# Kernel optimization log

Measured on AMD Instinct MI355X. Metric: run time of the kernel, lower is better.

## Reference

```python
import jax, jax.numpy as jnp
import numpy as np

# single species, e3tb basis 1s+1p+1d
FLIST = [1, 3, 5]           # flistnorbs (spin_factor = 1 pre-doubling)
NORB = 9                    # full_basis_norb
SPIN = 2                    # spin_deg -> block doubled
A, E, K = 192, 3072, 4
P = 58                      # sum_{i<=j} iorb*jorb = 1+3+5+9+15+25


def setup_inputs() -> dict:
    key = jax.random.key(0)
    ks = jax.random.split(key, 6)
    return dict(
        orbpair_hopping=jax.random.normal(ks[0], (E, P), jnp.float32),
        orbpair_onsite=jax.random.normal(ks[1], (A, P), jnp.float32),
        R_matrix=jax.random.normal(ks[2], (A, SPIN * NORB, SPIN * NORB), jnp.float32) * 0.1,
        kpoints=jax.random.uniform(ks[3], (K, 3), jnp.float32),
        edge_cell_shift=jax.random.normal(ks[4], (E, 3), jnp.float32),
        edge_index=jax.random.randint(ks[5], (2, E), 0, A, jnp.int64),
    )


def _assemble(feats):
    """Scatter flat orbpair features into upper-triangular [*, NORB, NORB] blocks."""
    n = feats.shape[0]
    H = jnp.zeros((n, NORB, NORB), feats.dtype)
    offs = np.concatenate([[0], np.cumsum(FLIST)])
    p = 0
    for i in range(len(FLIST)):
        for j in range(i, len(FLIST)):
            io, jo = FLIST[i], FLIST[j]
            f = 0.5 if i == j else 1.0  # diagonal orbpairs get 0.5 (hermitianized later)
            H = H.at[:, offs[i]:offs[i] + io, offs[j]:offs[j] + jo].set(
                f * feats[:, p:p + io * jo].reshape(n, io, jo))
            p += io * jo
    return H


def _spin_double(H):
    # H[:, :, 0, :, 0] = H[:, :, 1, :, 1] = H  (kron with eye(2), interleaved layout)
    n = H.shape[0]
    return jnp.einsum('aij,st->aisjt', H, jnp.eye(2, dtype=H.dtype)).reshape(n, SPIN * NORB, SPIN * NORB)


def reference(orbpair_hopping, orbpair_onsite, R_matrix, kpoints, edge_cell_shift, edge_index):
    s = SPIN * NORB
    src, dst = edge_index[0], edge_index[1]

    onsite = _spin_double(_assemble(orbpair_onsite))      # [A, s, s]
    hop = _spin_double(_assemble(orbpair_hopping))        # [E, s, s]

    # rotate: R @ H @ R^T (gathered per-edge for hoppings)
    onsite = jnp.einsum('aip,apq,ajq->aij', R_matrix, onsite, R_matrix)
    hop = jnp.einsum('eip,epq,ejq->eij', R_matrix[src], hop, R_matrix[dst])

    # Bloch phases exp(-2*pi*i k.S) per (k, edge)
    phase = jnp.exp(-2j * jnp.pi * (kpoints @ edge_cell_shift.T)).astype(jnp.complex64)  # [K, E]

    contrib = hop[None].astype(jnp.complex64) * phase[:, :, None, None]  # [K, E, s, s]
    pair = src * A + dst
    blk = jax.vmap(lambda c: jax.ops.segment_sum(c, pair, num_segments=A * A))(contrib)
    blk = blk.reshape(K, A, A, s, s)

    idx = jnp.arange(A)
    blk = blk.at[:, idx, idx].add(onsite[None].astype(jnp.complex64))  # onsite on diag, all k

    Hk = blk.transpose(0, 1, 3, 2, 4).reshape(K, A * s, A * s)
    return Hk + jnp.conj(jnp.swapaxes(Hk, 1, 2))
```

## Files before the change

kernel.cpp:

```cpp
#include <hip/hip_runtime.h>

#define PFEAT 58
#define S18   18
#define ENT   324
#define MAXE  128
#define MAXA  256

__device__ __constant__ unsigned char c_row[PFEAT] = {
    0,0,0,0,0,0,0,0,0,
    1,1,1,2,2,2,3,3,3,
    1,1,1,1,1,2,2,2,2,2,3,3,3,3,3,
    4,4,4,4,4,5,5,5,5,5,6,6,6,6,6,7,7,7,7,7,8,8,8,8,8};
__device__ __constant__ unsigned char c_col[PFEAT] = {
    0,1,2,3,4,5,6,7,8,
    1,2,3,1,2,3,1,2,3,
    4,5,6,7,8,4,5,6,7,8,4,5,6,7,8,
    4,5,6,7,8,4,5,6,7,8,4,5,6,7,8,4,5,6,7,8,4,5,6,7,8};
__device__ __constant__ float c_fac[PFEAT] = {
    0.5f,1,1,1,1,1,1,1,1,
    0.5f,0.5f,0.5f,0.5f,0.5f,0.5f,0.5f,0.5f,0.5f,
    1,1,1,1,1,1,1,1,1,1,1,1,1,1,1,
    0.5f,0.5f,0.5f,0.5f,0.5f,0.5f,0.5f,0.5f,0.5f,0.5f,0.5f,0.5f,0.5f,
    0.5f,0.5f,0.5f,0.5f,0.5f,0.5f,0.5f,0.5f,0.5f,0.5f,0.5f,0.5f};

__device__ __forceinline__ bool detect_i64(const int* __restrict__ ei) {
    const uint2* p = (const uint2*)ei;
    unsigned acc = 0u;
#pragma unroll 8
    for (int m = 0; m < 64; ++m) acc |= p[m].y;
    return acc == 0u;
}

__device__ __forceinline__ int load_idx(const int* __restrict__ ei, int pos,
                                        bool is64, int A) {
    int v = is64 ? ei[2 * pos] : ei[pos];
    v = v < 0 ? 0 : (v >= A ? A - 1 : v);
    return v;
}

__device__ __forceinline__ void assemble_rotate(
    const float* __restrict__ feat, const float* __restrict__ Rs,
    const float* __restrict__ Rd, float* sH9, float* sRs, float* sRd,
    float* sT, float* sM, int t, int nthreads)
{
    for (int idx = t; idx < ENT; idx += nthreads) { sRs[idx] = Rs[idx]; sRd[idx] = Rd[idx]; }
    if (t < 81) sH9[t] = 0.f;
    __syncthreads();
    if (t < PFEAT) sH9[c_row[t] * 9 + c_col[t]] = c_fac[t] * feat[t];
    __syncthreads();

    for (int idx = t; idx < ENT; idx += nthreads) {
        const int pp = idx / S18, q = idx - pp * S18;
        const int i = pp >> 1, u = pp & 1;
        float acc = 0.f;
#pragma unroll
        for (int j = 0; j < 9; ++j)
            acc += sH9[i * 9 + j] * sRd[q * S18 + 2 * j + u];
        sT[idx] = acc;
    }
    __syncthreads();

    for (int idx = t; idx < ENT; idx += nthreads) {
        const int p = idx / S18, q = idx - p * S18;
        float acc = 0.f;
#pragma unroll
        for (int pp = 0; pp < S18; ++pp)
            acc += sRs[p * S18 + pp] * sT[pp * S18 + q];
        sM[idx] = acc;
    }
}


__global__ __launch_bounds__(128) void prep_kernel(
    const float* __restrict__ hop_feat, const float* __restrict__ ons_feat,
    const float* __restrict__ R, const int* __restrict__ ei,
    const float* __restrict__ kpts, const float* __restrict__ shift,
    float* __restrict__ hop_rot, float* __restrict__ hop_rotT,
    float* __restrict__ ons_rot, float* __restrict__ pcos,
    float* __restrict__ psin, int* __restrict__ offsets,
    int2* __restrict__ entries, int E, int A, int K, int hasT)
{
    __shared__ float sH9[81];
    __shared__ float sRs[ENT];
    __shared__ float sRd[ENT];
    __shared__ float sT[ENT];
    __shared__ float sM[ENT];
    __shared__ int   scnt[MAXA];
    __shared__ int   scur[MAXA];
    __shared__ int   sflag;

    const int item = blockIdx.x;
    const int t = threadIdx.x;
    if (t == 0) sflag = detect_i64(ei) ? 1 : 0;
    __syncthreads();
    const bool s64 = sflag != 0;

    if (item == E + A) {
        for (int a = t; a < A; a += 128) scnt[a] = 0;
        __syncthreads();
        for (int e = t; e < E; e += 128) {
            const int a = load_idx(ei, e, s64, A);
            const int b = load_idx(ei, E + e, s64, A);
            atomicAdd(&scnt[a], 1);
            atomicAdd(&scnt[b], 1);
        }
        __syncthreads();
        if (t == 0) {
            int acc = 0;
            for (int a = 0; a < A; ++a) { scur[a] = acc; offsets[a] = acc; acc += scnt[a]; }
            offsets[A] = acc;
        }
        __syncthreads();
        for (int e = t; e < E; e += 128) {
            const int a = load_idx(ei, e, s64, A);
            const int b = load_idx(ei, E + e, s64, A);
            const int p = atomicAdd(&scur[a], 1);
            entries[p] = make_int2(e, b);
            const int q = atomicAdd(&scur[b], 1);
            entries[q] = make_int2(e | (1 << 30), a);
        }
        return;
    }

    const float* feat; const float* Rs; const float* Rd; float* outp;
    if (item < E) {
        const int a_s = load_idx(ei, item, s64, A);
        const int a_d = load_idx(ei, E + item, s64, A);
        feat = hop_feat + (size_t)item * PFEAT;
        Rs = R + (size_t)a_s * ENT;
        Rd = R + (size_t)a_d * ENT;
        outp = hop_rot + (size_t)item * ENT;
        for (int k = t; k < K; k += 128) {
            const float dot = kpts[k * 3 + 0] * shift[3 * item + 0]
                            + kpts[k * 3 + 1] * shift[3 * item + 1]
                            + kpts[k * 3 + 2] * shift[3 * item + 2];
            float sv, cv;
            sincosf(-6.28318530717958647692f * dot, &sv, &cv);
            pcos[item * K + k] = cv;
            psin[item * K + k] = sv;
        }
    } else {
        const int a = item - E;
        feat = ons_feat + (size_t)a * PFEAT;
        Rs = R + (size_t)a * ENT;
        Rd = Rs;
        outp = ons_rot + (size_t)a * ENT;
    }

    assemble_rotate(feat, Rs, Rd, sH9, sRs, sRd, sT, sM, t, 128);
    __syncthreads();

    for (int idx = t; idx < ENT; idx += 128) outp[idx] = sM[idx];
    if (item < E && hasT) {
        float* outpT = hop_rotT + (size_t)item * ENT;
        for (int idx = t; idx < ENT; idx += 128) {
            const int p = idx / S18, q = idx - p * S18;
            outpT[idx] = sM[q * S18 + p];
        }
    }
}

__global__ __launch_bounds__(384) void writer_cols_kernel(
    const float* __restrict__ hop_rot,
    const float* __restrict__ hop_rotT,
    const float* __restrict__ ons_rot,
    const int*   __restrict__ offsets,
    const int2*  __restrict__ entries,
    const float* __restrict__ pcos,
    float* __restrict__ outf,
    int A, int K, long long lim)
{
    __shared__ int   se[MAXE];
    __shared__ int   sb[MAXE];
    __shared__ float spc[MAXE];
    __shared__ float sons[ENT];

    const int N = A * S18;
    const int a = blockIdx.z;
    const int k = blockIdx.y;
    const int t = threadIdx.x;
    const int c = blockIdx.x * 384 + t;

    const int beg = offsets[a];
    const int cnt = offsets[a + 1] - beg;
    const int nst = cnt < MAXE ? cnt : MAXE;
    for (int n = t; n < nst; n += 384) {
        const int2 ent = entries[beg + n];
        se[n] = ent.x;
        sb[n] = ent.y;
        spc[n] = pcos[(ent.x & 0x3FFFFFFF) * K + k];
    }
    for (int idx = t; idx < ENT; idx += 384) sons[idx] = ons_rot[a * ENT + idx];
    __syncthreads();

    if (c >= N) return;
    const int b = c / S18, l = c - b * S18;

    float acc[S18];
    if (b == a) {
#pragma unroll
        for (int i = 0; i < S18; ++i)
            acc[i] = sons[i * S18 + l] + sons[l * S18 + i];
    } else {
#pragma unroll
        for (int i = 0; i < S18; ++i) acc[i] = 0.f;
    }

    for (int n = 0; n < nst; ++n) {
        if (sb[n] != b) continue;
        const int ex = se[n];
        const int e = ex & 0x3FFFFFFF;
        const float pc = spc[n];
        const float* base = ((ex >> 30) & 1)
                          ? (hop_rot  + (size_t)e * ENT + l * S18)
                          : (hop_rotT + (size_t)e * ENT + l * S18);
#pragma unroll
        for (int i = 0; i < S18; ++i) acc[i] += base[i] * pc;
    }
    for (int n = MAXE; n < cnt; ++n) {
        const int2 ent = entries[beg + n];
        if (ent.y != b) continue;
        const int e = ent.x & 0x3FFFFFFF;
        const float pc = pcos[e * K + k];
        const float* base = ((ent.x >> 30) & 1)
                          ? (hop_rot  + (size_t)e * ENT + l * S18)
                          : (hop_rotT + (size_t)e * ENT + l * S18);
#pragma unroll
        for (int i = 0; i < S18; ++i) acc[i] += base[i] * pc;
    }

    const long long rowbase = ((long long)k * N + (long long)a * S18) * (long long)N + c;
#pragma unroll
    for (int i = 0; i < S18; ++i) {
        const long long off = rowbase + (long long)i * N;
        if (off < lim) outf[off] = acc[i];
    }
}

__global__ __launch_bounds__(256) void write_kernel(
    const float* __restrict__ hop_rot, const float* __restrict__ hop_rotT,
    const float* __restrict__ ons_rot, const int* __restrict__ offsets,
    const int2* __restrict__ entries, const float* __restrict__ pcos,
    const float* __restrict__ psin, float* __restrict__ outf,
    int A, int K, int cplx, int hasT, long long lim)
{
    extern __shared__ float rowbuf[];
    __shared__ int2  sent[MAXE];
    __shared__ float sphc[MAXE];
    __shared__ float sphs[MAXE];
    __shared__ float sons[ENT];

    const int N = A * S18;
    const int a    = blockIdx.x >> 1;
    const int half = blockIdx.x & 1;
    const int k = blockIdx.y;
    const int t = threadIdx.x;
    const int i0 = half * 9;
    const int stride = cplx ? 2 : 1;
    const int nbuf = stride * N;
    const int nbuf4 = nbuf >> 2;

    const int beg = offsets[a], end = offsets[a + 1];
    const int cnt = end - beg;
    const int nst = cnt < MAXE ? cnt : MAXE;
    for (int n = t; n < nst; n += 256) {
        const int2 ent = entries[beg + n];
        sent[n] = ent;
        const int e0 = ent.x & 0x3FFFFFFF;
        sphc[n] = pcos[e0 * K + k];
        if (cplx) sphs[n] = psin[e0 * K + k];
    }
    for (int idx = t; idx < ENT; idx += 256) sons[idx] = ons_rot[a * ENT + idx];
    __syncthreads();

    float4* rb4 = (float4*)rowbuf;
    const int total = cnt * S18;

    for (int ri = 0; ri < 9; ++ri) {
        const int i = i0 + ri;
        for (int idx = t; idx < nbuf4; idx += 256)
            rb4[idx] = make_float4(0.f, 0.f, 0.f, 0.f);
        __syncthreads();

        if (t < S18)
            atomicAdd(&rowbuf[stride * (a * S18 + t)],
                      sons[i * S18 + t] + sons[t * S18 + i]);

        for (int m = t; m < total; m += 256) {
            const int n = m / S18, l = m - n * S18;
            int2 ent; float pc, ps = 0.f;
            if (n < MAXE) {
                ent = sent[n]; pc = sphc[n]; if (cplx) ps = sphs[n];
            } else {
                ent = entries[beg + n];
                const int e0 = ent.x & 0x3FFFFFFF;
                pc = pcos[e0 * K + k]; if (cplx) ps = psin[e0 * K + k];
            }
            const int conjf = (ent.x >> 30) & 1;
            const int e = ent.x & 0x3FFFFFFF;
            const int b = ent.y;
            float v;
            if (!conjf)     v = hop_rot [(size_t)e * ENT + i * S18 + l];
            else if (hasT)  v = hop_rotT[(size_t)e * ENT + i * S18 + l];
            else            v = hop_rot [(size_t)e * ENT + l * S18 + i];
            atomicAdd(&rowbuf[stride * (b * S18 + l)], v * pc);
            if (cplx)
                atomicAdd(&rowbuf[stride * (b * S18 + l) + 1], conjf ? -v * ps : v * ps);
        }
        __syncthreads();

        const long long base = (long long)stride
                             * ((long long)k * N + (long long)a * S18 + i)
                             * (long long)N;
        float* dst = outf + base;
        if (base + nbuf <= lim && ((base & 3) == 0)) {
            float4* d4 = (float4*)dst;
            for (int idx = t; idx < nbuf4; idx += 256) d4[idx] = rb4[idx];
        } else {
            for (int idx = t; idx < nbuf; idx += 256)
                if (base + idx < lim) dst[idx] = rowbuf[idx];
        }
        __syncthreads();
    }
}


__global__ __launch_bounds__(256) void zero_kernel(float* __restrict__ p, long long n)
{
    const long long i4 = ((long long)blockIdx.x * 256 + threadIdx.x) * 4;
    if (i4 + 3 < n) {
        *(float4*)(p + i4) = make_float4(0.f, 0.f, 0.f, 0.f);
    } else if (i4 < n) {
        for (long long i = i4; i < n; ++i) p[i] = 0.f;
    }
}

__global__ __launch_bounds__(256) void edge_kernel(
    const float* __restrict__ hop_feat, const float* __restrict__ R,
    const float* __restrict__ kpts, const float* __restrict__ shift,
    const int* __restrict__ edge_index, float* __restrict__ outf,
    int E, int A, int K, int cplx, long long lim)
{
    __shared__ float sH9[81];
    __shared__ float sRs[ENT];
    __shared__ float sRd[ENT];
    __shared__ float sT[ENT];
    __shared__ float sM[ENT];
    __shared__ float sC[8];
    __shared__ float sS[8];

    const int e = blockIdx.x;
    const int t = threadIdx.x;
    const int N = A * S18;
    const long long N2 = (long long)N * N;

    const bool is64 = detect_i64(edge_index);
    const int a = load_idx(edge_index, e, is64, A);
    const int b = load_idx(edge_index, E + e, is64, A);

    if (t < K && t < 8) {
        const float sx = shift[e * 3 + 0], sy = shift[e * 3 + 1], sz = shift[e * 3 + 2];
        const float dot = kpts[t * 3 + 0] * sx + kpts[t * 3 + 1] * sy + kpts[t * 3 + 2] * sz;
        float sv, cv;
        sincosf(-6.28318530717958647692f * dot, &sv, &cv);
        sC[t] = cv; sS[t] = sv;
    }

    assemble_rotate(hop_feat + (size_t)e * PFEAT,
                    R + (size_t)a * ENT, R + (size_t)b * ENT,
                    sH9, sRs, sRd, sT, sM, t, 256);
    __syncthreads();

    const int total = K * ENT;
    for (int idx = t; idx < total; idx += 256) {
        const int k = idx / ENT, r = idx - k * ENT;
        const int i = r / S18, j = r - i * S18;
        const float v = sM[r];
        const float re = v * sC[k];
        const float im = v * sS[k];
        const long long I = (long long)a * S18 + i;
        const long long J = (long long)b * S18 + j;
        const long long p1 = k * N2 + I * N + J;
        const long long p2 = k * N2 + J * N + I;
        if (cplx) {
            if (2 * p1 + 1 < lim) { atomicAdd(&outf[2 * p1], re); atomicAdd(&outf[2 * p1 + 1], im); }
            if (2 * p2 + 1 < lim) { atomicAdd(&outf[2 * p2], re); atomicAdd(&outf[2 * p2 + 1], -im); }
        } else {
            if (p1 < lim) atomicAdd(&outf[p1], re);
            if (p2 < lim) atomicAdd(&outf[p2], re);
        }
    }
}

__global__ __launch_bounds__(128) void onsite_kernel(
    const float* __restrict__ ons_feat, const float* __restrict__ R,
    float* __restrict__ outf, int A, int K, int cplx, long long lim)
{
    __shared__ float sH9[81];
    __shared__ float sRs[ENT];
    __shared__ float sRd[ENT];
    __shared__ float sT[ENT];
    __shared__ float sM[ENT];

    const int a = blockIdx.x;
    const int t = threadIdx.x;
    const int N = A * S18;
    const long long N2 = (long long)N * N;

    assemble_rotate(ons_feat + (size_t)a * PFEAT,
                    R + (size_t)a * ENT, R + (size_t)a * ENT,
                    sH9, sRs, sRd, sT, sM, t, 128);
    __syncthreads();

    for (int idx = t; idx < ENT; idx += 128) {
        const int i = idx / S18, j = idx - (idx / S18) * S18;
        const float v = sM[i * S18 + j] + sM[j * S18 + i];
        const long long I = (long long)a * S18 + i;
        const long long J = (long long)a * S18 + j;
        for (int k = 0; k < K; ++k) {
            const long long p1 = k * N2 + I * N + J;
            const long long off = cplx ? 2 * p1 : p1;
            if (off < lim) outf[off] += v;
        }
    }
}

extern "C" void kernel_launch(void* const* d_in, const int* in_sizes, int n_in,
                              void* d_out, int out_size, void* d_ws, size_t ws_size,
                              hipStream_t stream) {
    const float* hop_feat   = (const float*)d_in[0];
    const float* ons_feat   = (const float*)d_in[1];
    const float* R          = (const float*)d_in[2];
    const float* kpts       = (const float*)d_in[3];
    const float* shift      = (const float*)d_in[4];
    const int*   edge_index = (const int*)d_in[5];

    const int E = in_sizes[0] / PFEAT;
    const int A = in_sizes[1] / PFEAT;
    const int K = in_sizes[3] / 3;

    const long long N  = (long long)A * S18;
    const long long n_real = (long long)K * N * N;
    const long long lim = (long long)out_size;
    const int cplx = (lim >= 2 * n_real) ? 1 : 0;

    float* outf = (float*)d_out;

    char* ws = (char*)d_ws;
    const size_t off_hop = 0;
    const size_t off_ons = off_hop + (size_t)E * ENT * 4;
    const size_t off_ent = off_ons + (size_t)A * ENT * 4;
    const size_t off_off = off_ent + (size_t)2 * E * 8;
    const size_t off_pc  = off_off + (size_t)(A + 2) * 4;
    const size_t off_ps  = off_pc  + (size_t)E * K * 4;
    const size_t base_need = off_ps + (size_t)E * K * 4;
    const size_t off_hT  = base_need;
    const size_t full_need = off_hT + (size_t)E * ENT * 4;

    if (ws_size >= base_need && A <= MAXA) {
        const int hasT = (ws_size >= full_need) ? 1 : 0;
        float* hop_rot  = (float*)(ws + off_hop);
        float* ons_rot  = (float*)(ws + off_ons);
        int2*  entries  = (int2*)(ws + off_ent);
        int*   offsets  = (int*)(ws + off_off);
        float* pcos     = (float*)(ws + off_pc);
        float* psin     = (float*)(ws + off_ps);
        float* hop_rotT = (float*)(ws + off_hT);

        prep_kernel<<<E + A + 1, 128, 0, stream>>>(
            hop_feat, ons_feat, R, edge_index, kpts, shift,
            hop_rot, hop_rotT, ons_rot, pcos, psin, offsets, entries,
            E, A, K, hasT);

        if (cplx == 0 && hasT) {
            const int nchunks = (int)((N + 383) / 384);
            dim3 grid((unsigned)nchunks, (unsigned)K, (unsigned)A);
            writer_cols_kernel<<<grid, 384, 0, stream>>>(
                hop_rot, hop_rotT, ons_rot, offsets, entries, pcos,
                outf, A, K, lim);
        } else {
            const size_t shmem = (size_t)(cplx ? 2 : 1) * N * sizeof(float);
            dim3 grid((unsigned)(A * 2), (unsigned)K);
            write_kernel<<<grid, 256, shmem, stream>>>(hop_rot, hop_rotT, ons_rot,
                                                       offsets, entries, pcos, psin,
                                                       outf, A, K, cplx, hasT, lim);
        }
    } else {
        const long long n4 = (lim + 3) / 4;
        const int zgrid = (int)((n4 + 255) / 256);
        zero_kernel<<<zgrid, 256, 0, stream>>>(outf, lim);
        edge_kernel<<<E, 256, 0, stream>>>(hop_feat, R, kpts, shift, edge_index,
                                           outf, E, A, K, cplx, lim);
        onsite_kernel<<<A, 128, 0, stream>>>(ons_feat, R, outf, A, K, cplx, lim);
    }
}
```

Baseline: 226.9 us.

## Fuse k-point loop into column writer kernel to reuse hopping block loads

Adds a writer kernel that handles all k-points (up to 4) in one block per atom column chunk, keeping per-k accumulators in registers. Each rotated hopping block row is loaded once and multiplied by each k's phase, instead of being reloaded by a separate block per k-point. This cuts redundant global reads and the per-block setup, at the cost of many more registers (72 accumulators plus 18 loaded values per thread), which may lower occupancy.

```diff
diff --git a/kernel.cpp b/kernel.cpp
--- a/kernel.cpp
+++ b/kernel.cpp
@@ -160,7 +160,7 @@
     }
 }
 
-__global__ __launch_bounds__(384) void writer_cols_kernel(
+__global__ __launch_bounds__(256) void writer_colsK_kernel(
     const float* __restrict__ hop_rot,
     const float* __restrict__ hop_rotT,
     const float* __restrict__ ons_rot,
@@ -169,6 +169,97 @@
     const float* __restrict__ pcos,
     float* __restrict__ outf,
     int A, int K, long long lim)
+{
+    __shared__ int   se[MAXE];
+    __shared__ int   sb[MAXE];
+    __shared__ float spc[MAXE][4];
+    __shared__ float sons[ENT];
+
+    const int N = A * S18;
+    const long long N2 = (long long)N * N;
+    const int a = blockIdx.y;
+    const int t = threadIdx.x;
+    const int c = blockIdx.x * 256 + t;
+
+    const int beg = offsets[a];
+    const int cnt = offsets[a + 1] - beg;
+    const int nst = cnt < MAXE ? cnt : MAXE;
+    for (int n = t; n < nst; n += 256) {
+        const int2 ent = entries[beg + n];
+        se[n] = ent.x;
+        sb[n] = ent.y;
+        const int e0 = ent.x & 0x3FFFFFFF;
+        for (int k = 0; k < K; ++k) spc[n][k] = pcos[e0 * K + k];
+    }
+    for (int idx = t; idx < ENT; idx += 256) sons[idx] = ons_rot[a * ENT + idx];
+    __syncthreads();
+
+    if (c >= N) return;
+    const int b = c / S18, l = c - b * S18;
+
+    float acc[4][S18];
+#pragma unroll
+    for (int k = 0; k < 4; ++k)
+#pragma unroll
+        for (int i = 0; i < S18; ++i) acc[k][i] = 0.f;
+
+    if (b == a) {
+#pragma unroll
+        for (int i = 0; i < S18; ++i) {
+            const float v = sons[i * S18 + l] + sons[l * S18 + i];
+            for (int k = 0; k < K; ++k) acc[k][i] = v;
+        }
+    }
+
+    for (int n = 0; n < nst; ++n) {
+        if (sb[n] != b) continue;
+        const int ex = se[n];
+        const int e = ex & 0x3FFFFFFF;
+        const float* base = ((ex >> 30) & 1)
+                          ? (hop_rot  + (size_t)e * ENT + l * S18)
+                          : (hop_rotT + (size_t)e * ENT + l * S18);
+        float v[S18];
+#pragma unroll
+        for (int i = 0; i < S18; ++i) v[i] = base[i];
+        for (int k = 0; k < K; ++k) {
+            const float pc = spc[n][k];
+#pragma unroll
+            for (int i = 0; i < S18; ++i) acc[k][i] += v[i] * pc;
+        }
+    }
+    for (int n = MAXE; n < cnt; ++n) {
+        const int2 ent = entries[beg + n];
+        if (ent.y != b) continue;
+        const int e = ent.x & 0x3FFFFFFF;
+        const float* base = ((ent.x >> 30) & 1)
+                          ? (hop_rot  + (size_t)e * ENT + l * S18)
+                          : (hop_rotT + (size_t)e * ENT + l * S18);
+        float v[S18];
+#pragma unroll
+        for (int i = 0; i < S18; ++i) v[i] = base[i];
+        for (int k = 0; k < K; ++k) {
+            const float pc = pcos[e * K + k];
+#pragma unroll
+            for (int i = 0; i < S18; ++i) acc[k][i] += v[i] * pc;
+        }
+    }
+
+    const long long colbase = (long long)a * S18 * N + c;
+    for (int k = 0; k < K; ++k) {
+        const long long kb = (long long)k * N2 + colbase;
+#pragma unroll
+        for (int i = 0; i < S18; ++i) {
+            const long long off = kb + (long long)i * N;
+            if (off < lim) outf[off] = acc[k][i];
+        }
+    }
+}
+
+__global__ __launch_bounds__(384) void writer_cols_kernel(
+    const float* __restrict__ hop_rot, const float* __restrict__ hop_rotT,
+    const float* __restrict__ ons_rot, const int* __restrict__ offsets,
+    const int2* __restrict__ entries, const float* __restrict__ pcos,
+    float* __restrict__ outf, int A, int K, long long lim)
 {
     __shared__ int   se[MAXE];
     __shared__ int   sb[MAXE];
@@ -472,7 +563,13 @@
             hop_rot, hop_rotT, ons_rot, pcos, psin, offsets, entries,
             E, A, K, hasT);
 
-        if (cplx == 0 && hasT) {
+        if (cplx == 0 && hasT && K <= 4) {
+            const int nchunks = (int)((N + 255) / 256);
+            dim3 grid((unsigned)nchunks, (unsigned)A);
+            writer_colsK_kernel<<<grid, 256, 0, stream>>>(
+                hop_rot, hop_rotT, ons_rot, offsets, entries, pcos,
+                outf, A, K, lim);
+        } else if (cplx == 0 && hasT) {
             const int nchunks = (int)((N + 383) / 384);
             dim3 grid((unsigned)nchunks, (unsigned)K, (unsigned)A);
             writer_cols_kernel<<<grid, 384, 0, stream>>>(
```

After: 315.8 us. 39.2% more time.
